# Kernel optimization log

Hardware: AMD Instinct MI355X
Metric: run time of the kernel (lower is better)

Reference implementation:

```python
import jax, jax.numpy as jnp
import numpy as np

NS = 50000   # number of source cells
NT = 50000   # number of target cells
E = 1_600_000  # nnz of neighborhood (avg degree 32)
DIN = 64
DOUT = 64


def setup_inputs() -> dict:
    key = jax.random.key(0)
    ks = jax.random.split(key, 14)
    w_scale = ((2.0 / (DIN + DOUT)) ** 0.5) * 1.414  # xavier_uniform-ish std with gain
    a_scale = (1.0 / (3 * DOUT)) ** 0.5
    nrm = lambda k, s, sc: jax.random.normal(k, s, jnp.float32) * sc
    return {
        "x_source": jax.random.normal(ks[0], (NS, DIN), jnp.float32),
        "x_target": jax.random.normal(ks[1], (NT, DIN), jnp.float32),
        "nb_rows": jax.random.randint(ks[2], (E,), 0, NT, jnp.int32),   # target index of each nnz
        "nb_cols": jax.random.randint(ks[3], (E,), 0, NS, jnp.int32),   # source index of each nnz
        "nb_vals": jax.random.uniform(ks[4], (E,), jnp.float32),        # neighborhood values
        "cci_vals": jax.random.uniform(ks[5], (E,), jnp.float32),       # cci values (same pattern)
        "w_s": nrm(ks[6], (DIN, DOUT), w_scale),
        "w_t": nrm(ks[7], (DIN, DOUT), w_scale),
        "w_s_cci": nrm(ks[8], (DIN, DOUT), w_scale),   # shared: ParameterList([p]*2) aliases one param
        "w_t_cci": nrm(ks[9], (DIN, DOUT), w_scale),
        "src_W": nrm(ks[10], (3, 3 * DOUT, DOUT), a_scale),
        "src_b": jnp.zeros((3, DOUT), jnp.float32),
        "tgt_W": nrm(ks[11], (3, 3 * DOUT, DOUT), a_scale),
        "tgt_b": jnp.zeros((3, DOUT), jnp.float32),
    }


def _pna(seg, nbr, vals, m, W, b, n_seg):
    """PNA aggregation over a sparse neighborhood given as an edge list.
    seg: [E] destination segment ids; nbr: [E] neighbor ids into m; vals: [E] edge weights.
    Aggregators: weighted sum, mean (by neighbor count), max; then Linear(3D -> D)."""
    g = m[nbr] * vals[:, None]                                   # [E, D]
    s_sum = jax.ops.segment_sum(g, seg, num_segments=n_seg)      # [n_seg, D]
    cnt = jax.ops.segment_sum(jnp.ones_like(vals), seg, num_segments=n_seg)
    s_mean = s_sum / jnp.maximum(cnt, 1.0)[:, None]
    s_max = jax.ops.segment_max(g, seg, num_segments=n_seg)
    s_max = jnp.where(jnp.isfinite(s_max), s_max, 0.0)           # empty segments -> 0
    return jnp.concatenate([s_sum, s_mean, s_max], axis=-1) @ W + b


def reference(x_source, x_target, nb_rows, nb_cols, nb_vals, cci_vals,
              w_s, w_t, w_s_cci, w_t_cci, src_W, src_b, tgt_W, tgt_b):
    n_s, n_t = x_source.shape[0], x_target.shape[0]
    # dense projections (w_s_cci / w_t_cci are shared between the two cci branches)
    s_msg = x_source @ w_s          # [NS, DOUT]
    s_msg2 = x_source @ w_s_cci     # used for both cci branches
    t_msg = x_target @ w_t          # [NT, DOUT]
    t_msg2 = x_target @ w_t_cci
    had_vals = cci_vals * nb_vals   # sparse hadamard (same pattern)

    # message on source: aggregate target features along transposed neighborhood [NS, NT]
    msg_src = (_pna(nb_cols, nb_rows, nb_vals, t_msg, src_W[0], src_b[0], n_s)
               + _pna(nb_cols, nb_rows, cci_vals, t_msg2, src_W[1], src_b[1], n_s)
               + _pna(nb_cols, nb_rows, had_vals, t_msg2, src_W[2], src_b[2], n_s))
    # message on target: aggregate source features along neighborhood [NT, NS]
    msg_tgt = (_pna(nb_rows, nb_cols, nb_vals, s_msg, tgt_W[0], tgt_b[0], n_t)
               + _pna(nb_rows, nb_cols, cci_vals, s_msg2, tgt_W[1], tgt_b[1], n_t)
               + _pna(nb_rows, nb_cols, had_vals, s_msg2, tgt_W[2], tgt_b[2], n_t))
    # update_func is None -> return raw messages
    return msg_src, msg_tgt
```

## Files before the change

kernel.cpp:

```cpp
#include <hip/hip_runtime.h>
#include <hip/hip_bf16.h>

typedef unsigned int u32;
typedef unsigned short u16;
typedef __attribute__((ext_vector_type(8))) short short8;
typedef __attribute__((ext_vector_type(4))) float f32x4;

__device__ __forceinline__ u32 f2bf(float f){
  u32 u = __float_as_uint(f);
  return (u + 0x7fffu + ((u >> 16) & 1u)) >> 16;
}
__device__ __forceinline__ float bflo(u32 p){ return __uint_as_float(p << 16); }
__device__ __forceinline__ float bfhi(u32 p){ return __uint_as_float(p & 0xffff0000u); }

__global__ __launch_bounds__(256) void proj_kernel(
    const float* __restrict__ xs, const float* __restrict__ xt,
    const float* __restrict__ w_s, const float* __restrict__ w_t,
    const float* __restrict__ w_s_cci, const float* __restrict__ w_t_cci,
    u32* __restrict__ mS, u32* __restrict__ mT, int ns, int nt)
{
  __shared__ float wa[4096], wb[4096];
  const int dir = blockIdx.y;
  const float* x  = dir ? xt : xs;
  const float* wA = dir ? w_t : w_s;
  const float* wB = dir ? w_t_cci : w_s_cci;
  u32* out = dir ? mT : mS;
  const int n = dir ? nt : ns;
  const int tid = threadIdx.x;
  for (int i = tid; i < 4096; i += 256){ wa[i] = wA[i]; wb[i] = wB[i]; }
  __syncthreads();
  const int wid = tid >> 6, lane = tid & 63;
  for (int row = blockIdx.x*4 + wid; row < n; row += gridDim.x*4){
    float xv = x[(size_t)row*64 + lane];
    float accA = 0.f, accB = 0.f;
    #pragma unroll
    for (int k = 0; k < 64; k++){
      float xk = __shfl(xv, k, 64);
      accA = fmaf(xk, wa[k*64 + lane], accA);
      accB = fmaf(xk, wb[k*64 + lane], accB);
    }
    out[(size_t)row*64 + lane] = f2bf(accA) | (f2bf(accB) << 16);
  }
}

__global__ __launch_bounds__(256) void wprep_kernel(
  const float* __restrict__ srcW, const float* __restrict__ tgtW,
  u16* __restrict__ WtS, u16* __restrict__ WtT)
{
  int idx = blockIdx.x*256 + threadIdx.x;
  if (idx < 576*64){
    int col = idx / 576, k = idx - col*576;
    WtS[idx] = (u16)f2bf(srcW[(size_t)k*64 + col]);
    WtT[idx] = (u16)f2bf(tgtW[(size_t)k*64 + col]);
  }
}

__global__ __launch_bounds__(256) void hist_kernel(
  const int* __restrict__ rows, const int* __restrict__ cols,
  int* cntR, int* cntC, int E)
{
  int e = blockIdx.x*256 + threadIdx.x;
  if (e < E){
    atomicAdd(&cntR[rows[e]], 1);
    atomicAdd(&cntC[cols[e]], 1);
  }
}

__global__ __launch_bounds__(1024) void scan_kernel(
  const int* __restrict__ cntC, const int* __restrict__ cntR,
  int* ptrC, int* ptrR, int* curC, int* curR, int ns, int nt)
{
  __shared__ int lds[1024];
  const int* cnt; int* ptr; int* cur; int n;
  if (blockIdx.x == 0){ cnt=cntC; ptr=ptrC; cur=curC; n=ns; }
  else                { cnt=cntR; ptr=ptrR; cur=curR; n=nt; }
  const int t = threadIdx.x;
  const int C = (n + 1023) / 1024;
  const int base = t*C;
  int s = 0;
  for (int i = 0; i < C; i++){ int idx = base+i; if (idx < n) s += cnt[idx]; }
  lds[t] = s; __syncthreads();
  for (int off = 1; off < 1024; off <<= 1){
    int v = 0; if (t >= off) v = lds[t-off];
    __syncthreads();
    lds[t] += v;
    __syncthreads();
  }
  int run = lds[t] - s;
  for (int i = 0; i < C; i++){
    int idx = base+i;
    if (idx < n){ ptr[idx] = run; cur[idx] = run; run += cnt[idx]; }
  }
  if (t == 1023) ptr[n] = lds[1023];
}

__global__ __launch_bounds__(256) void scatter_kernel(
  const int* __restrict__ rows, const int* __restrict__ cols,
  const float* __restrict__ nbv, const float* __restrict__ ccv,
  int* curR, int* curC,
  int* nbrT, float* w0T, float* w1T,
  int* nbrS, float* w0S, float* w1S, int E)
{
  int e = blockIdx.x*256 + threadIdx.x;
  if (e < E){
    int r = rows[e], c = cols[e];
    float a = nbv[e], b = ccv[e];
    int pT = atomicAdd(&curR[r], 1);
    nbrT[pT] = c; w0T[pT] = a; w1T[pT] = b;
    int pS = atomicAdd(&curC[c], 1);
    nbrS[pS] = r; w0S[pS] = a; w1S[pS] = b;
  }
}

__global__ __launch_bounds__(256) void agg_kernel(
  const int* __restrict__ ptrC, const int* __restrict__ ptrR,
  const int* __restrict__ nbrS, const float* __restrict__ w0S, const float* __restrict__ w1S,
  const int* __restrict__ nbrT, const float* __restrict__ w0T, const float* __restrict__ w1T,
  const u32* __restrict__ mS, const u32* __restrict__ mT,
  u16* __restrict__ statsS, u16* __restrict__ statsT, int ns, int nt)
{
  const int dir = blockIdx.y;
  const int nseg = dir ? nt : ns;
  const int* ptr = dir ? ptrR : ptrC;
  const int* nbr = dir ? nbrT : nbrS;
  const float* w0 = dir ? w0T : w0S;
  const float* w1 = dir ? w1T : w1S;
  const u32* mtab = dir ? mS : mT;
  u16* stats = dir ? statsT : statsS;

  const int wid = threadIdx.x >> 6, lane = threadIdx.x & 63;
  const int seg = blockIdx.x*4 + wid;
  if (seg >= nseg) return;
  const int beg = ptr[seg], end = ptr[seg+1];

  float s0=0.f, s1=0.f, s2=0.f;
  float mx0=-INFINITY, mx1=-INFINITY, mx2=-INFINITY;

  int e = beg;
  for (; e + 4 <= end; e += 4){
    int n4[4]; float a4[4], b4[4]; u32 p4[4];
    #pragma unroll
    for (int u=0;u<4;u++){ n4[u]=nbr[e+u]; a4[u]=w0[e+u]; b4[u]=w1[e+u]; }
    #pragma unroll
    for (int u=0;u<4;u++){ p4[u] = mtab[(size_t)n4[u]*64 + lane]; }
    #pragma unroll
    for (int u=0;u<4;u++){
      float g0 = bflo(p4[u]) * a4[u];
      float g1 = bfhi(p4[u]) * b4[u];
      float g2 = g1 * a4[u];
      s0 += g0; s1 += g1; s2 += g2;
      mx0 = fmaxf(mx0, g0); mx1 = fmaxf(mx1, g1); mx2 = fmaxf(mx2, g2);
    }
  }
  for (; e < end; e++){
    int nb = nbr[e]; float a = w0[e], b = w1[e];
    u32 p = mtab[(size_t)nb*64 + lane];
    float g0 = bflo(p) * a;
    float g1 = bfhi(p) * b;
    float g2 = g1 * a;
    s0 += g0; s1 += g1; s2 += g2;
    mx0 = fmaxf(mx0, g0); mx1 = fmaxf(mx1, g1); mx2 = fmaxf(mx2, g2);
  }
  if (end == beg){ mx0 = 0.f; mx1 = 0.f; mx2 = 0.f; }

  size_t o = (size_t)seg*384 + lane;
  stats[o      ] = (u16)f2bf(s0);
  stats[o + 64 ] = (u16)f2bf(s1);
  stats[o + 128] = (u16)f2bf(s2);
  stats[o + 192] = (u16)f2bf(mx0);
  stats[o + 256] = (u16)f2bf(mx1);
  stats[o + 320] = (u16)f2bf(mx2);
}

#define HROW 584

__global__ __launch_bounds__(256) void lin_kernel(
  const u16* __restrict__ statsS, const u16* __restrict__ statsT,
  const int* __restrict__ ptrC, const int* __restrict__ ptrR,
  const u16* __restrict__ WtS, const u16* __restrict__ WtT,
  const float* __restrict__ srcB, const float* __restrict__ tgtB,
  float* __restrict__ outp, int ns, int nt)
{
  __shared__ u16 h[64*HROW];
  __shared__ float invc[64];
  const int dir = blockIdx.y;
  const u16* stats = dir ? statsT : statsS;
  const int* ptr   = dir ? ptrR : ptrC;
  const u16* Wt    = dir ? WtT : WtS;
  const float* Bg  = dir ? tgtB : srcB;
  const int n = dir ? nt : ns;
  float* out = outp + (dir ? (size_t)ns*64 : 0);
  const int tid = threadIdx.x;
  const int wv = tid >> 6, lane = tid & 63;
  const int seg0 = blockIdx.x * 64;
  if (seg0 >= n) return;

  const int bcol = wv*16 + (lane & 15);
  const int krow = (lane >> 4) * 8;
  short8 bfrag[18];
  #pragma unroll
  for (int t = 0; t < 18; t++)
    bfrag[t] = *(const short8*)&Wt[(size_t)bcol*576 + t*32 + krow];

  if (tid < 64){
    int seg = seg0 + tid;
    float c = (seg < n) ? (float)(ptr[seg+1] - ptr[seg]) : 1.f;
    invc[tid] = 1.f / fmaxf(c, 1.f);
  }
  __syncthreads();

  for (int idx = tid; idx < 64*192; idx += 256){
    int s = idx / 192, i = idx - s*192;
    int blk = i >> 5, cp = (i & 31) * 2;
    int seg = seg0 + s;
    u32 v = 0;
    if (seg < n) v = *(const u32*)&stats[(size_t)seg*384 + blk*64 + cp];
    u32* hrow = (u32*)&h[s*HROW];
    if (blk < 3){
      hrow[(blk*192 + cp) >> 1] = v;
      float ic = invc[s];
      hrow[(blk*192 + 64 + cp) >> 1] = f2bf(bflo(v)*ic) | (f2bf(bfhi(v)*ic) << 16);
    } else {
      hrow[((blk-3)*192 + 128 + cp) >> 1] = v;
    }
  }
  __syncthreads();

  f32x4 acc[4] = {};
  const int arow = lane & 15;
  #pragma unroll
  for (int t = 0; t < 18; t++){
    #pragma unroll
    for (int rb = 0; rb < 4; rb++){
      short8 a = *(const short8*)&h[(rb*16 + arow)*HROW + t*32 + krow];
      acc[rb] = __builtin_amdgcn_mfma_f32_16x16x32_bf16(a, bfrag[t], acc[rb], 0, 0, 0);
    }
  }

  float bv = Bg[bcol] + Bg[64 + bcol] + Bg[128 + bcol];
  #pragma unroll
  for (int rb = 0; rb < 4; rb++){
    #pragma unroll
    for (int r = 0; r < 4; r++){
      int seg = seg0 + rb*16 + (lane >> 4)*4 + r;
      if (seg < n) out[(size_t)seg*64 + bcol] = acc[rb][r] + bv;
    }
  }
}

extern "C" void kernel_launch(void* const* d_in, const int* in_sizes, int n_in,
                              void* d_out, int out_size, void* d_ws, size_t ws_size,
                              hipStream_t stream)
{
  const float* xs   = (const float*)d_in[0];
  const float* xt   = (const float*)d_in[1];
  const int*   rows = (const int*)  d_in[2];
  const int*   cols = (const int*)  d_in[3];
  const float* nbv  = (const float*)d_in[4];
  const float* ccv  = (const float*)d_in[5];
  const float* w_s  = (const float*)d_in[6];
  const float* w_t  = (const float*)d_in[7];
  const float* w_sc = (const float*)d_in[8];
  const float* w_tc = (const float*)d_in[9];
  const float* srcW = (const float*)d_in[10];
  const float* srcB = (const float*)d_in[11];
  const float* tgtW = (const float*)d_in[12];
  const float* tgtB = (const float*)d_in[13];
  const int ns = in_sizes[0] / 64;
  const int nt = in_sizes[1] / 64;
  const int E  = in_sizes[4];

  char* ws = (char*)d_ws;
  size_t off = 0;
  auto alloc = [&](size_t bytes)->char* {
    char* p = ws + off;
    off = (off + bytes + 255) & ~(size_t)255;
    return p;
  };
  u32* mS    = (u32*)alloc((size_t)ns*64*4);
  u32* mT    = (u32*)alloc((size_t)nt*64*4);
  int* cntC  = (int*)alloc((size_t)(ns+nt)*4);
  int* cntR  = cntC + ns;
  int* ptrC  = (int*)alloc((size_t)(ns+1)*4);
  int* ptrR  = (int*)alloc((size_t)(nt+1)*4);
  int* curC  = (int*)alloc((size_t)ns*4);
  int* curR  = (int*)alloc((size_t)nt*4);
  int*   nbrS = (int*)  alloc((size_t)E*4);
  float* w0S  = (float*)alloc((size_t)E*4);
  float* w1S  = (float*)alloc((size_t)E*4);
  int*   nbrT = (int*)  alloc((size_t)E*4);
  float* w0T  = (float*)alloc((size_t)E*4);
  float* w1T  = (float*)alloc((size_t)E*4);
  u16* statsS = (u16*)alloc((size_t)ns*384*2);
  u16* statsT = (u16*)alloc((size_t)nt*384*2);
  u16* WtS    = (u16*)alloc((size_t)576*64*2);
  u16* WtT    = (u16*)alloc((size_t)576*64*2);

  hipMemsetAsync(cntC, 0, (size_t)(ns+nt)*4, stream);
  proj_kernel<<<dim3(128,2), 256, 0, stream>>>(xs,xt,w_s,w_t,w_sc,w_tc,mS,mT,ns,nt);
  wprep_kernel<<<(576*64 + 255)/256, 256, 0, stream>>>(srcW,tgtW,WtS,WtT);
  hist_kernel<<<(E+255)/256, 256, 0, stream>>>(rows,cols,cntR,cntC,E);
  scan_kernel<<<2, 1024, 0, stream>>>(cntC,cntR,ptrC,ptrR,curC,curR,ns,nt);
  scatter_kernel<<<(E+255)/256, 256, 0, stream>>>(rows,cols,nbv,ccv,curR,curC,
                                                  nbrT,w0T,w1T,nbrS,w0S,w1S,E);
  const int mseg = (ns > nt ? ns : nt);
  agg_kernel<<<dim3((mseg+3)/4, 2), 256, 0, stream>>>(ptrC,ptrR,nbrS,w0S,w1S,
                                                      nbrT,w0T,w1T,mS,mT,statsS,statsT,ns,nt);
  lin_kernel<<<dim3((mseg+63)/64, 2), 256, 0, stream>>>(statsS,statsT,ptrC,ptrR,
                                                        WtS,WtT,srcB,tgtB,
                                                        (float*)d_out,ns,nt);
}
```

Baseline: 854.5 us.

## Split aggregation into column slices with four edges per wave and sliced stats layout

The aggregation kernel now splits the 64 feature columns into four 16-column slices, one slice per grid z index. Each wave processes four edges at once, one per 16-lane group, then reduces the partial sums and maxes across groups with shuffles. Neighbor indices and weights are software-prefetched one step ahead with nontemporal loads. Stats are written in a slice-major layout that the linear kernel reads with adjusted indexing. The aim is more memory-level parallelism and smaller per-wave working sets for the gathers. In exchange, the edge metadata is read four times (once per slice), each gather is only 64 bytes wide, and shuffle reductions are added.

```diff
diff --git a/kernel.cpp b/kernel.cpp
--- a/kernel.cpp
+++ b/kernel.cpp
@@ -3,6 +3,7 @@
 
 typedef unsigned int u32;
 typedef unsigned short u16;
+typedef unsigned long long u64;
 typedef __attribute__((ext_vector_type(8))) short short8;
 typedef __attribute__((ext_vector_type(4))) float f32x4;
 
@@ -119,7 +120,8 @@
   const u32* __restrict__ mS, const u32* __restrict__ mT,
   u16* __restrict__ statsS, u16* __restrict__ statsT, int ns, int nt)
 {
-  const int dir = blockIdx.y;
+  const int z = blockIdx.z;
+  const int dir = z >> 2, slice = z & 3;
   const int nseg = dir ? nt : ns;
   const int* ptr = dir ? ptrR : ptrC;
   const int* nbr = dir ? nbrT : nbrS;
@@ -133,43 +135,60 @@
   if (seg >= nseg) return;
   const int beg = ptr[seg], end = ptr[seg+1];
 
+  const int egrp = lane >> 4;
+  const int col = slice*16 + (lane & 15);
+
   float s0=0.f, s1=0.f, s2=0.f;
   float mx0=-INFINITY, mx1=-INFINITY, mx2=-INFINITY;
 
-  int e = beg;
-  for (; e + 4 <= end; e += 4){
-    int n4[4]; float a4[4], b4[4]; u32 p4[4];
-    #pragma unroll
-    for (int u=0;u<4;u++){ n4[u]=nbr[e+u]; a4[u]=w0[e+u]; b4[u]=w1[e+u]; }
-    #pragma unroll
-    for (int u=0;u<4;u++){ p4[u] = mtab[(size_t)n4[u]*64 + lane]; }
-    #pragma unroll
-    for (int u=0;u<4;u++){
-      float g0 = bflo(p4[u]) * a4[u];
-      float g1 = bfhi(p4[u]) * b4[u];
-      float g2 = g1 * a4[u];
+  int e = beg + egrp;
+  bool v = e < end;
+  int nb = 0; float a = 0.f, b = 0.f;
+  if (v){
+    nb = __builtin_nontemporal_load(&nbr[e]);
+    a  = __builtin_nontemporal_load(&w0[e]);
+    b  = __builtin_nontemporal_load(&w1[e]);
+  }
+  while (__any(v)){
+    int e2 = e + 4;
+    bool v2 = e2 < end;
+    int nb2 = 0; float a2 = 0.f, b2 = 0.f;
+    if (v2){
+      nb2 = __builtin_nontemporal_load(&nbr[e2]);
+      a2  = __builtin_nontemporal_load(&w0[e2]);
+      b2  = __builtin_nontemporal_load(&w1[e2]);
+    }
+    if (v){
+      u32 f = mtab[(size_t)nb*64 + col];
+      float g0 = bflo(f) * a;
+      float g1 = bfhi(f) * b;
+      float g2 = g1 * a;
       s0 += g0; s1 += g1; s2 += g2;
       mx0 = fmaxf(mx0, g0); mx1 = fmaxf(mx1, g1); mx2 = fmaxf(mx2, g2);
     }
-  }
-  for (; e < end; e++){
-    int nb = nbr[e]; float a = w0[e], b = w1[e];
-    u32 p = mtab[(size_t)nb*64 + lane];
-    float g0 = bflo(p) * a;
-    float g1 = bfhi(p) * b;
-    float g2 = g1 * a;
-    s0 += g0; s1 += g1; s2 += g2;
-    mx0 = fmaxf(mx0, g0); mx1 = fmaxf(mx1, g1); mx2 = fmaxf(mx2, g2);
+    v = v2; e = e2; nb = nb2; a = a2; b = b2;
+  }
+
+  #pragma unroll
+  for (int d = 16; d <= 32; d <<= 1){
+    s0 += __shfl_xor(s0, d, 64);
+    s1 += __shfl_xor(s1, d, 64);
+    s2 += __shfl_xor(s2, d, 64);
+    mx0 = fmaxf(mx0, __shfl_xor(mx0, d, 64));
+    mx1 = fmaxf(mx1, __shfl_xor(mx1, d, 64));
+    mx2 = fmaxf(mx2, __shfl_xor(mx2, d, 64));
   }
   if (end == beg){ mx0 = 0.f; mx1 = 0.f; mx2 = 0.f; }
 
-  size_t o = (size_t)seg*384 + lane;
-  stats[o      ] = (u16)f2bf(s0);
-  stats[o + 64 ] = (u16)f2bf(s1);
-  stats[o + 128] = (u16)f2bf(s2);
-  stats[o + 192] = (u16)f2bf(mx0);
-  stats[o + 256] = (u16)f2bf(mx1);
-  stats[o + 320] = (u16)f2bf(mx2);
+  if (lane < 16){
+    size_t base = ((size_t)slice*nseg + seg)*96 + (lane & 15);
+    __builtin_nontemporal_store((u16)f2bf(s0),  &stats[base      ]);
+    __builtin_nontemporal_store((u16)f2bf(s1),  &stats[base + 16 ]);
+    __builtin_nontemporal_store((u16)f2bf(s2),  &stats[base + 32 ]);
+    __builtin_nontemporal_store((u16)f2bf(mx0), &stats[base + 48 ]);
+    __builtin_nontemporal_store((u16)f2bf(mx1), &stats[base + 64 ]);
+    __builtin_nontemporal_store((u16)f2bf(mx2), &stats[base + 80 ]);
+  }
 }
 
 #define HROW 584
@@ -214,7 +233,8 @@
     int blk = i >> 5, cp = (i & 31) * 2;
     int seg = seg0 + s;
     u32 v = 0;
-    if (seg < n) v = *(const u32*)&stats[(size_t)seg*384 + blk*64 + cp];
+    if (seg < n)
+      v = *(const u32*)&stats[((size_t)(cp >> 4)*n + seg)*96 + blk*16 + (cp & 15)];
     u32* hrow = (u32*)&h[s*HROW];
     if (blk < 3){
       hrow[(blk*192 + cp) >> 1] = v;
@@ -304,8 +324,9 @@
   scatter_kernel<<<(E+255)/256, 256, 0, stream>>>(rows,cols,nbv,ccv,curR,curC,
                                                   nbrT,w0T,w1T,nbrS,w0S,w1S,E);
   const int mseg = (ns > nt ? ns : nt);
-  agg_kernel<<<dim3((mseg+3)/4, 2), 256, 0, stream>>>(ptrC,ptrR,nbrS,w0S,w1S,
-                                                      nbrT,w0T,w1T,mS,mT,statsS,statsT,ns,nt);
+  agg_kernel<<<dim3((mseg+3)/4, 1, 8), 256, 0, stream>>>(ptrC,ptrR,nbrS,w0S,w1S,
+                                                         nbrT,w0T,w1T,mS,mT,
+                                                         statsS,statsT,ns,nt);
   lin_kernel<<<dim3((mseg+63)/64, 2), 256, 0, stream>>>(statsS,statsT,ptrC,ptrR,
                                                         WtS,WtT,srcB,tgtB,
                                                         (float*)d_out,ns,nt);
```

Result: slower. 1.269 ms (+48.5%).
